# Performance work log

Hardware: AMD Instinct MI355X
Metric: run time of the kernel (lower is better)

Reference implementation:

```python
import jax, jax.numpy as jnp
import numpy as np

B = 2048   # batch size
D = 2048   # feature dim (ResNet-50)
H = 2048   # projection hidden dim
T = 0.1    # temperature
EPS_BN = 1e-5
CC_ITERS = 32  # >= ~2*log2(B), enough for pointer-jumping convergence


def setup_inputs() -> dict:
    key = jax.random.key(0)
    ks = jax.random.split(key, 4)
    s = 0.02
    return {
        "x1": jax.random.normal(ks[0], (B, D), dtype=jnp.float32),
        "x2": jax.random.normal(ks[1], (B, D), dtype=jnp.float32),
        "W1": jax.random.normal(ks[2], (H, D), dtype=jnp.float32) * s,
        "b1": jnp.zeros((H,), jnp.float32),
        "gamma": jnp.ones((H,), jnp.float32),
        "beta": jnp.zeros((H,), jnp.float32),
        "W2": jax.random.normal(ks[3], (D, H), dtype=jnp.float32) * s,
        "b2": jnp.zeros((D,), jnp.float32),
    }


def _head(x, W1, b1, gamma, beta, W2, b2):
    # ProjectionHead: Linear -> BatchNorm1d (train mode, batch stats) -> ReLU -> Linear
    h = x @ W1.T + b1
    mu = h.mean(0)
    var = h.var(0)  # biased variance, as torch BN uses for normalization
    h = (h - mu) * jax.lax.rsqrt(var + EPS_BN) * gamma + beta
    h = jax.nn.relu(h)
    o = h @ W2.T + b2
    n = jnp.maximum(jnp.linalg.norm(o, axis=1, keepdims=True), 1e-12)
    return o / n  # F.normalize


def _cc_mask(feat):
    # build_connected_component: kNN(k=1) graph + connected components -> same-label mask
    b = feat.shape[0]
    sim = jax.lax.stop_gradient(feat @ feat.T) - 2.0 * jnp.eye(b, dtype=feat.dtype)
    y = jnp.argmax(sim, axis=1)  # topk(1) neighbor per row
    # min-label propagation with pointer jumping (GPU-native union-find equivalent)
    def body(_, l):
        ln = jnp.minimum(l, l[y])      # propagate along edge i -> y[i]
        ln = ln.at[y].min(l)           # propagate along reverse edge y[i] -> i
        return jnp.minimum(ln, ln[ln])  # pointer jumping
    labels = jax.lax.fori_loop(0, CC_ITERS, body, jnp.arange(b))
    return (labels[:, None] == labels[None, :]).astype(feat.dtype)


def _sup_contra(logits, mask, diag):
    dm = 1.0 - diag
    mask = mask * dm
    exp_logits = jnp.exp(logits) * dm
    log_prob = logits - jnp.log(exp_logits.sum(1, keepdims=True))
    mean_log_prob_pos = (mask * log_prob).sum(1) / mask.sum(1)
    return (-mean_log_prob_pos).mean()


def reference(x1, x2, W1, b1, gamma, beta, W2, b2):
    # Only head2 branch contributes to the returned graph_loss (head1 branch is dead code
    # w.r.t. the return value), so we compute exactly the graph_loss path.
    feat1 = _head(x1, W1, b1, gamma, beta, W2, b2)
    feat2 = _head(x2, W1, b1, gamma, beta, W2, b2)
    mask1 = _cc_mask(feat1)
    mask2 = _cc_mask(feat2)
    diag = jnp.eye(B, dtype=feat1.dtype)
    loss = _sup_contra(feat1 @ feat1.T / T, mask2, diag)
    loss = loss + _sup_contra(feat2 @ feat2.T / T, mask1, diag)
    return loss / 2.0
```

## Files before the change

kernel.cpp:

```cpp
#include <hip/hip_runtime.h>
#include <hip/hip_bf16.h>

typedef __bf16 bf16_t;
typedef __bf16 bf16x4 __attribute__((ext_vector_type(4)));
typedef __bf16 bf16x8 __attribute__((ext_vector_type(8)));
typedef float  f32x4  __attribute__((ext_vector_type(4)));

__device__ __forceinline__ void gload_lds16(const void* g, void* l)
{
    __builtin_amdgcn_global_load_lds((__attribute__((address_space(1))) void*)g,
                                     (__attribute__((address_space(3))) void*)l,
                                     16, 0, 0);
}

__global__ __launch_bounds__(256) void cast_all(const float* __restrict__ x1, const float* __restrict__ x2,
                                                const float* __restrict__ W1, const float* __restrict__ W2,
                                                bf16_t* __restrict__ xcatb, bf16_t* __restrict__ W1b,
                                                bf16_t* __restrict__ W2b)
{
    const size_t i  = ((size_t)blockIdx.x * 256 + threadIdx.x) * 4;
    const size_t M4 = 1ull << 22;
    const size_t r  = i >> 22;
    const size_t off = i & (M4 - 1);
    const float* src; bf16_t* dst;
    if (r == 0)      { src = x1; dst = xcatb; }
    else if (r == 1) { src = x2; dst = xcatb + M4; }
    else if (r == 2) { src = W1; dst = W1b; }
    else             { src = W2; dst = W2b; }
    f32x4 v = *(const f32x4*)(src + off);
    bf16x4 o;
    o[0] = (bf16_t)v[0]; o[1] = (bf16_t)v[1]; o[2] = (bf16_t)v[2]; o[3] = (bf16_t)v[3];
    *(bf16x4*)(dst + off) = o;
}

__global__ __launch_bounds__(256) void gemm_bt(
    const bf16_t* __restrict__ A, const bf16_t* __restrict__ B,
    const float* __restrict__ bias, void* __restrict__ Cv,
    int N, int K, int rows_per_batch, long long b_batch_stride,
    int mode, int c_bf16,
    float* __restrict__ ps, float* __restrict__ ps2,
    float* __restrict__ rsq, const float* __restrict__ rnv,
    unsigned long long* __restrict__ pkey, float* __restrict__ lseP)
{
    __shared__ bf16_t lsA[128 * 64];
    __shared__ bf16_t lsB[128 * 64];
    __shared__ float  cs2[4][64];
    __shared__ float  cq2[4][64];
    __shared__ float  rq2[4][64];
    __shared__ float  ls2[4][64];
    __shared__ unsigned long long kv2[4][64];
    const int tid  = threadIdx.x;
    const int lane = tid & 63;
    const int wave = tid >> 6;
    const int wm   = (wave >> 1) * 64;
    const int wn   = (wave & 1) * 64;
    const int m0   = blockIdx.y * 128;
    const int n0   = blockIdx.x * 128;
    const bf16_t* Bb = B + (long long)(m0 / rows_per_batch) * b_batch_stride;

    f32x4 acc[4][4] = {};

    const int srow = tid >> 3;
    const int scol = (tid & 7) * 8;
    for (int kt = 0; kt < K; kt += 64) {
#pragma unroll
        for (int i = 0; i < 4; ++i) {
            const int r = i * 32 + srow;
            gload_lds16(A  + (size_t)(m0 + r) * K + kt + scol, lsA + r * 64 + scol);
            gload_lds16(Bb + (size_t)(n0 + r) * K + kt + scol, lsB + r * 64 + scol);
        }
        __syncthreads();
#pragma unroll
        for (int ks = 0; ks < 2; ++ks) {
            const int kk = ks * 32 + (lane >> 4) * 8;
            bf16x8 af[4], bfr[4];
#pragma unroll
            for (int f = 0; f < 4; ++f) {
                af[f]  = *(const bf16x8*)&lsA[(wm + f * 16 + (lane & 15)) * 64 + kk];
                bfr[f] = *(const bf16x8*)&lsB[(wn + f * 16 + (lane & 15)) * 64 + kk];
            }
#pragma unroll
            for (int fm = 0; fm < 4; ++fm)
#pragma unroll
                for (int fn = 0; fn < 4; ++fn)
                    acc[fm][fn] = __builtin_amdgcn_mfma_f32_16x16x32_bf16(af[fm], bfr[fn], acc[fm][fn], 0, 0, 0);
        }
        __syncthreads();
    }

    if (mode == 2) {
        const int rnb = (m0 >> 11) * 2048;
#pragma unroll
        for (int fm = 0; fm < 4; ++fm) {
            const int mb = m0 + wm + fm * 16 + ((lane >> 4) << 2);
            const f32x4 rm = *(const f32x4*)&rnv[mb];
#pragma unroll
            for (int fn = 0; fn < 4; ++fn) {
                const float rc = rnv[rnb + n0 + wn + fn * 16 + (lane & 15)];
#pragma unroll
                for (int r = 0; r < 4; ++r)
                    acc[fm][fn][r] *= rm[r] * rc;
            }
        }
    }

#pragma unroll
    for (int fm = 0; fm < 4; ++fm) {
        const int rb = m0 + wm + fm * 16 + ((lane >> 4) << 2);
#pragma unroll
        for (int fn = 0; fn < 4; ++fn) {
            const int colg = n0 + wn + fn * 16 + (lane & 15);
            const float bv = bias ? bias[colg] : 0.0f;
            if (c_bf16) {
                bf16_t* Cb = (bf16_t*)Cv;
#pragma unroll
                for (int r = 0; r < 4; ++r)
                    Cb[(size_t)(rb + r) * N + colg] = (bf16_t)(acc[fm][fn][r] + bv);
            } else {
                float* Cf = (float*)Cv;
#pragma unroll
                for (int r = 0; r < 4; ++r)
                    Cf[(size_t)(rb + r) * N + colg] = acc[fm][fn][r] + bv;
            }
        }
    }

    if (mode == 1) {
#pragma unroll
        for (int fn = 0; fn < 4; ++fn) {
            const int cl = fn * 16 + (lane & 15);
            const float bv = bias[n0 + wn + cl];
            float s = 0.f, q = 0.f;
#pragma unroll
            for (int fm = 0; fm < 4; ++fm)
#pragma unroll
                for (int r = 0; r < 4; ++r) {
                    const float v = acc[fm][fn][r] + bv;
                    s += v; q += v * v;
                }
            s += __shfl_xor(s, 16); q += __shfl_xor(q, 16);
            s += __shfl_xor(s, 32); q += __shfl_xor(q, 32);
            if (lane < 16) { cs2[wave][cl] = s; cq2[wave][cl] = q; }
        }
        __syncthreads();
        if (tid < 128) {
            const int wlo = (tid < 64) ? 0 : 1;
            const int cl  = tid & 63;
            ps [(size_t)blockIdx.y * 2048 + n0 + tid] = cs2[wlo][cl] + cs2[wlo + 2][cl];
            ps2[(size_t)blockIdx.y * 2048 + n0 + tid] = cq2[wlo][cl] + cq2[wlo + 2][cl];
        }
    } else if (mode == 3) {
#pragma unroll
        for (int fm = 0; fm < 4; ++fm)
#pragma unroll
            for (int r = 0; r < 4; ++r) {
                float q = 0.f;
#pragma unroll
                for (int fn = 0; fn < 4; ++fn) {
                    const float v = acc[fm][fn][r] + bias[n0 + wn + fn * 16 + (lane & 15)];
                    q += v * v;
                }
                q += __shfl_xor(q, 1); q += __shfl_xor(q, 2);
                q += __shfl_xor(q, 4); q += __shfl_xor(q, 8);
                if ((lane & 15) == 0)
                    rq2[wave][fm * 16 + ((lane >> 4) << 2) + r] = q;
            }
        __syncthreads();
        if (tid < 128) {
            const int wlo = (tid < 64) ? 0 : 2;
            const int rl  = tid & 63;
            rsq[(size_t)blockIdx.x * 4096 + m0 + tid] = rq2[wlo][rl] + rq2[wlo + 1][rl];
        }
    } else if (mode == 2) {
#pragma unroll
        for (int fm = 0; fm < 4; ++fm)
#pragma unroll
            for (int r = 0; r < 4; ++r) {
                const int rl   = fm * 16 + ((lane >> 4) << 2) + r;
                const int self = (m0 + wm + rl) & 2047;
                float best = -1.0e38f; int bi = 0x7fffffff; float se = 0.f;
#pragma unroll
                for (int fn = 0; fn < 4; ++fn) {
                    const int cg = n0 + wn + fn * 16 + (lane & 15);
                    const float v = acc[fm][fn][r];
                    if (cg != self) {
                        se += expf(10.0f * v);
                        if (v > best) { best = v; bi = cg; }
                    }
                }
#pragma unroll
                for (int st = 1; st <= 8; st <<= 1) {
                    const float ov = __shfl_xor(best, st);
                    const int   oi = __shfl_xor(bi, st);
                    if (ov > best || (ov == best && oi < bi)) { best = ov; bi = oi; }
                    se += __shfl_xor(se, st);
                }
                if ((lane & 15) == 0) {
                    unsigned u = __float_as_uint(best);
                    u = (u & 0x80000000u) ? ~u : (u | 0x80000000u);
                    kv2[wave][rl] = ((unsigned long long)u << 32) | (unsigned)(~bi);
                    ls2[wave][rl] = se;
                }
            }
        __syncthreads();
        if (tid < 128) {
            const int wlo = (tid < 64) ? 0 : 2;
            const int rl  = tid & 63;
            const unsigned long long a = kv2[wlo][rl], b = kv2[wlo + 1][rl];
            pkey[(size_t)blockIdx.x * 4096 + m0 + tid] = a > b ? a : b;
            lseP[(size_t)blockIdx.x * 4096 + m0 + tid] = ls2[wlo][rl] + ls2[wlo + 1][rl];
        }
    }
}

__global__ __launch_bounds__(256) void bn_final2(const float* __restrict__ ps, const float* __restrict__ ps2,
                                                 float* __restrict__ mu, float* __restrict__ rinv)
{
    const int c = blockIdx.x * 256 + threadIdx.x;
    const int b = c >> 11, col = c & 2047;
    float s = 0.f, s2 = 0.f;
    for (int i = 0; i < 16; ++i) {
        s  += ps [(size_t)(b * 16 + i) * 2048 + col];
        s2 += ps2[(size_t)(b * 16 + i) * 2048 + col];
    }
    const float m = s * (1.0f / 2048.0f);
    const float v = s2 * (1.0f / 2048.0f) - m * m;
    mu[c]   = m;
    rinv[c] = rsqrtf(v + 1e-5f);
}

__global__ __launch_bounds__(256) void bn_apply(const bf16_t* __restrict__ h, const float* __restrict__ mu,
                                                const float* __restrict__ rinv, const float* __restrict__ gamma,
                                                const float* __restrict__ beta, bf16_t* __restrict__ out)
{
    const size_t base = ((size_t)blockIdx.x * 256 + threadIdx.x) * 8;
    const int col = (int)(base & 2047);
    const int br  = (int)(base >> 22);
    bf16x8 v = *(const bf16x8*)(h + base);
    bf16x8 o;
#pragma unroll
    for (int j = 0; j < 8; ++j) {
        const int c = col + j;
        const float f = (float)v[j];
        const float t = (f - mu[br * 2048 + c]) * rinv[br * 2048 + c] * gamma[c] + beta[c];
        o[j] = (bf16_t)fmaxf(t, 0.0f);
    }
    *(bf16x8*)(out + base) = o;
}

__global__ __launch_bounds__(256) void norm_final(const float* __restrict__ rsq, float* __restrict__ rn)
{
    const int r = blockIdx.x * 256 + threadIdx.x;
    float s = 0.f;
    for (int nb = 0; nb < 16; ++nb) s += rsq[(size_t)nb * 4096 + r];
    rn[r] = 1.0f / fmaxf(sqrtf(s), 1e-12f);
}

__global__ __launch_bounds__(1024) void cc_labels(const unsigned long long* __restrict__ pkey,
                                                  int* __restrict__ labg)
{
    __shared__ int A_[2048];
    __shared__ int Bn[2048];
    __shared__ int Y_[2048];
    __shared__ int chg;
    const int br = blockIdx.x;
    const int t = threadIdx.x;
    if (t == 0) chg = 0;
    for (int i = t; i < 2048; i += 1024) {
        const int row = br * 2048 + i;
        unsigned long long k = 0ull;
        for (int nb = 0; nb < 16; ++nb) {
            const unsigned long long v = pkey[(size_t)nb * 4096 + row];
            k = (v > k) ? v : k;
        }
        Y_[i] = (int)~((unsigned)(k & 0xFFFFFFFFull));
        A_[i] = i;
    }
    __syncthreads();
    for (int it = 0; it < 32; ++it) {
        for (int i = t; i < 2048; i += 1024) Bn[i] = min(A_[i], A_[Y_[i]]);
        __syncthreads();
        for (int i = t; i < 2048; i += 1024) atomicMin(&Bn[Y_[i]], A_[i]);
        __syncthreads();
        int ch = 0;
        for (int i = t; i < 2048; i += 1024) {
            const int b = Bn[i];
            const int nv = min(b, Bn[b]);
            if (nv != A_[i]) { ch = 1; A_[i] = nv; }
        }
        if (ch) atomicOr(&chg, 1);
        __syncthreads();
        const int c = chg;
        __syncthreads();
        if (t == 0) chg = 0;
        if (!c) break;
    }
    for (int i = t; i < 2048; i += 1024) labg[br * 2048 + i] = A_[i];
}

__global__ __launch_bounds__(256) void loss_rows(const bf16_t* __restrict__ simb, const int* __restrict__ labels,
                                                 const float* __restrict__ lseP, float* __restrict__ terms)
{
    const int row = blockIdx.x;
    const int br  = row >> 11;
    const int* lab = labels + ((1 - br) << 11);
    const int self = row & 2047;
    const int li = lab[self];
    const int t = threadIdx.x;
    const bf16x8 v8 = *(const bf16x8*)(simb + (size_t)row * 2048 + t * 8);
    float psum = 0.f; int pc = 0;
#pragma unroll
    for (int j = 0; j < 8; ++j) {
        const int c = t * 8 + j;
        if (c == self) continue;
        if (lab[c] == li) { psum += 10.0f * (float)v8[j]; pc++; }
    }
    __shared__ float PS[256]; __shared__ int PC[256];
    PS[t] = psum; PC[t] = pc;
    __syncthreads();
    for (int off = 128; off; off >>= 1) {
        if (t < off) { PS[t] += PS[t + off]; PC[t] += PC[t + off]; }
        __syncthreads();
    }
    if (t == 0) {
        float se = 0.f;
        for (int nb = 0; nb < 16; ++nb) se += lseP[(size_t)nb * 4096 + row];
        terms[row] = logf(se) - PS[0] / (float)PC[0];
    }
}

__global__ __launch_bounds__(1024) void final_reduce(const float* __restrict__ terms, float* __restrict__ out)
{
    const int t = threadIdx.x;
    float s = terms[t] + terms[t + 1024] + terms[t + 2048] + terms[t + 3072];
    __shared__ float S[1024];
    S[t] = s;
    __syncthreads();
    for (int off = 512; off; off >>= 1) { if (t < off) S[t] += S[t + off]; __syncthreads(); }
    if (t == 0) out[0] = S[0] * (1.0f / 4096.0f);
}

extern "C" void kernel_launch(void* const* d_in, const int* in_sizes, int n_in,
                              void* d_out, int out_size, void* d_ws, size_t ws_size,
                              hipStream_t stream)
{
    const float* x1    = (const float*)d_in[0];
    const float* x2    = (const float*)d_in[1];
    const float* W1    = (const float*)d_in[2];
    const float* b1    = (const float*)d_in[3];
    const float* gamma = (const float*)d_in[4];
    const float* beta  = (const float*)d_in[5];
    const float* W2    = (const float*)d_in[6];
    const float* b2    = (const float*)d_in[7];

    char* ws = (char*)d_ws;
    const size_t MB = 1024ull * 1024ull;
    const size_t NN = 2048ull * 2048ull;
    bf16_t* W1b    = (bf16_t*)(ws + 0);
    bf16_t* W2b    = (bf16_t*)(ws + 8 * MB);
    bf16_t* xcatb  = (bf16_t*)(ws + 16 * MB);
    bf16_t* hnb    = (bf16_t*)(ws + 16 * MB);
    bf16_t* hb16   = (bf16_t*)(ws + 32 * MB);
    bf16_t* ob16   = (bf16_t*)(ws + 64 * MB);
    bf16_t* simb   = (bf16_t*)(ws + 0);
    float*  psA    = (float*)(ws + 80 * MB);
    float*  psB    = psA + 32 * 2048;
    float*  rsq    = psB + 32 * 2048;
    float*  mu     = rsq + 16 * 4096;
    float*  rinv   = mu + 4096;
    float*  rn     = rinv + 4096;
    float*  lseP   = rn + 4096;
    unsigned long long* pkey = (unsigned long long*)(lseP + 16 * 4096);
    int*    labels = (int*)(pkey + 16 * 4096);
    float*  terms  = (float*)(labels + 4096);

    cast_all<<<16384, 256, 0, stream>>>(x1, x2, W1, W2, xcatb, W1b, W2b);

    gemm_bt<<<dim3(16, 32), 256, 0, stream>>>(xcatb, W1b, b1, hb16, 2048, 2048, 1 << 30, 0,
                                              1, 1, psA, psB, nullptr, nullptr, nullptr, nullptr);
    bn_final2<<<16, 256, 0, stream>>>(psA, psB, mu, rinv);
    bn_apply<<<4096, 256, 0, stream>>>(hb16, mu, rinv, gamma, beta, hnb);

    gemm_bt<<<dim3(16, 32), 256, 0, stream>>>(hnb, W2b, b2, ob16, 2048, 2048, 1 << 30, 0,
                                              3, 1, nullptr, nullptr, rsq, nullptr, nullptr, nullptr);
    norm_final<<<16, 256, 0, stream>>>(rsq, rn);

    gemm_bt<<<dim3(16, 32), 256, 0, stream>>>(ob16, ob16, nullptr, simb, 2048, 2048, 2048, (long long)NN,
                                              2, 1, nullptr, nullptr, nullptr, rn, pkey, lseP);

    cc_labels<<<2, 1024, 0, stream>>>(pkey, labels);
    loss_rows<<<4096, 256, 0, stream>>>(simb, labels, lseP, terms);
    final_reduce<<<1, 1024, 0, stream>>>(terms, (float*)d_out);
}
```

Measured before the change: 238.8 us.

## Add 256x256-tile 8-wave pipelined GEMM for the first projection layer

Replaces the generic 128x128 gemm_bt for the first linear layer (4096x2048x2048) with a dedicated 512-thread kernel that uses 256x256 tiles, a 4-stage LDS ring of K=32 slices with XOR swizzle, and interleaved global-to-LDS prefetch with MFMA blocks under barriers and setprio. Larger tiles raise arithmetic intensity and the deeper pipeline is meant to hide load latency. The BN partial-sum reduction moves into the new kernel, and bn_final2 now sums 8 row-block partials instead of 16. The costs are 128 blocks on a large GPU (under one wave of CUs), higher register pressure, and a schedule that relies on hand-tuned waitcnt counts.

```diff
diff --git a/kernel.cpp b/kernel.cpp
--- a/kernel.cpp
+++ b/kernel.cpp
@@ -33,19 +33,162 @@
     *(bf16x4*)(dst + off) = o;
 }
 
+__global__ __launch_bounds__(512, 2) void gemm8(
+    const bf16_t* __restrict__ A, const bf16_t* __restrict__ B,
+    const float* __restrict__ bias, bf16_t* __restrict__ C,
+    float* __restrict__ ps, float* __restrict__ ps2)
+{
+    __shared__ bf16_t lsA[4][256 * 32];
+    __shared__ bf16_t lsB[4][256 * 32];
+    __shared__ float  cs2[8][64], cq2[8][64];
+    const int tid  = threadIdx.x;
+    const int lane = tid & 63;
+    const int wave = tid >> 6;
+    const int l15  = lane & 15;
+    const int cg   = lane >> 4;
+    const int wm   = (wave >> 2) * 128;
+    const int wn   = (wave & 3) * 64;
+    const int m0   = blockIdx.y * 256;
+    const int n0   = blockIdx.x * 256;
+    const int K = 2048, N = 2048, NT = 32;
+
+    f32x4 acc[8][4] = {};
+
+    auto STAGE = [&](const bf16_t* __restrict__ G, int row0, int k0, bf16_t* dst) {
+#pragma unroll
+        for (int i = 0; i < 2; ++i) {
+            const int ch  = wave * 128 + i * 64 + lane;
+            const int row = ch >> 2;
+            const int cs  = (ch & 3) ^ (row & 3);
+            gload_lds16(G + (size_t)(row0 + row) * K + k0 + cs * 8,
+                        dst + wave * 1024 + i * 512 + lane * 8);
+        }
+    };
+    auto FRAG = [&](const bf16_t* u, int row) -> bf16x8 {
+        return *(const bf16x8*)&u[row * 32 + ((cg ^ (row & 3)) << 3)];
+    };
+    auto LOADA = [&](const bf16_t* uA, int g, bf16x8* af) {
+#pragma unroll
+        for (int j = 0; j < 4; ++j) af[j] = FRAG(uA, wm + (g * 4 + j) * 16 + l15);
+    };
+    auto LOADB = [&](const bf16_t* uB, bf16x8* bfr) {
+#pragma unroll
+        for (int j = 0; j < 4; ++j) bfr[j] = FRAG(uB, wn + j * 16 + l15);
+    };
+    auto DOMFMA = [&](int g, bf16x8* af, bf16x8* bfr) {
+        __builtin_amdgcn_s_setprio(1);
+#pragma unroll
+        for (int j = 0; j < 4; ++j)
+#pragma unroll
+            for (int fn = 0; fn < 4; ++fn)
+                acc[g * 4 + j][fn] =
+                    __builtin_amdgcn_mfma_f32_16x16x32_bf16(af[j], bfr[fn], acc[g * 4 + j][fn], 0, 0, 0);
+        __builtin_amdgcn_s_setprio(0);
+    };
+
+    STAGE(A, m0, 0,  lsA[0]);
+    STAGE(B, n0, 0,  lsB[0]);
+    STAGE(A, m0, 32, lsA[1]);
+    STAGE(B, n0, 32, lsB[1]);
+    asm volatile("s_waitcnt vmcnt(4)" ::: "memory");
+    __builtin_amdgcn_sched_barrier(0);
+    __builtin_amdgcn_s_barrier();
+
+    for (int t = 0; t < NT; ++t) {
+        const int s0 = (2 * t) & 3, s1 = (2 * t + 1) & 3;
+        const int s2 = (2 * t + 2) & 3, s3 = (2 * t + 3) & 3;
+        const bool st = (t < NT - 1);
+        const int kn = (t + 1) * 64;
+        bf16x8 af[4], bfr[4];
+
+        LOADB(lsB[s0], bfr);
+        LOADA(lsA[s0], 0, af);
+        if (st) STAGE(A, m0, kn, lsA[s2]);
+        __builtin_amdgcn_sched_barrier(0);
+        __builtin_amdgcn_s_barrier();
+        __builtin_amdgcn_sched_barrier(0);
+        DOMFMA(0, af, bfr);
+        __builtin_amdgcn_sched_barrier(0);
+        __builtin_amdgcn_s_barrier();
+
+        LOADA(lsA[s0], 1, af);
+        if (st) { STAGE(B, n0, kn, lsB[s2]);
+                  asm volatile("s_waitcnt vmcnt(4)" ::: "memory"); }
+        else      asm volatile("s_waitcnt vmcnt(0)" ::: "memory");
+        __builtin_amdgcn_sched_barrier(0);
+        __builtin_amdgcn_s_barrier();
+        __builtin_amdgcn_sched_barrier(0);
+        DOMFMA(1, af, bfr);
+        __builtin_amdgcn_sched_barrier(0);
+        __builtin_amdgcn_s_barrier();
+
+        LOADB(lsB[s1], bfr);
+        LOADA(lsA[s1], 0, af);
+        if (st) STAGE(A, m0, kn + 32, lsA[s3]);
+        __builtin_amdgcn_sched_barrier(0);
+        __builtin_amdgcn_s_barrier();
+        __builtin_amdgcn_sched_barrier(0);
+        DOMFMA(0, af, bfr);
+        __builtin_amdgcn_sched_barrier(0);
+        __builtin_amdgcn_s_barrier();
+
+        LOADA(lsA[s1], 1, af);
+        if (st) { STAGE(B, n0, kn + 32, lsB[s3]);
+                  asm volatile("s_waitcnt vmcnt(4)" ::: "memory"); }
+        __builtin_amdgcn_sched_barrier(0);
+        __builtin_amdgcn_s_barrier();
+        __builtin_amdgcn_sched_barrier(0);
+        DOMFMA(1, af, bfr);
+        __builtin_amdgcn_sched_barrier(0);
+        __builtin_amdgcn_s_barrier();
+    }
+
+#pragma unroll
+    for (int fm = 0; fm < 8; ++fm) {
+        const int rb = m0 + wm + fm * 16 + ((lane >> 4) << 2);
+#pragma unroll
+        for (int fn = 0; fn < 4; ++fn) {
+            const int colg = n0 + wn + fn * 16 + l15;
+            const float bv = bias[colg];
+#pragma unroll
+            for (int r = 0; r < 4; ++r)
+                C[(size_t)(rb + r) * N + colg] = (bf16_t)(acc[fm][fn][r] + bv);
+        }
+    }
+#pragma unroll
+    for (int fn = 0; fn < 4; ++fn) {
+        const int cl = fn * 16 + l15;
+        const float bv = bias[n0 + wn + cl];
+        float s = 0.f, q = 0.f;
+#pragma unroll
+        for (int fm = 0; fm < 8; ++fm)
+#pragma unroll
+            for (int r = 0; r < 4; ++r) {
+                const float v = acc[fm][fn][r] + bv;
+                s += v; q += v * v;
+            }
+        s += __shfl_xor(s, 16); q += __shfl_xor(q, 16);
+        s += __shfl_xor(s, 32); q += __shfl_xor(q, 32);
+        if (lane < 16) { cs2[wave][cl] = s; cq2[wave][cl] = q; }
+    }
+    __syncthreads();
+    if (tid < 256) {
+        const int qn = tid >> 6, cl = tid & 63;
+        ps [(size_t)blockIdx.y * 2048 + n0 + tid] = cs2[qn][cl] + cs2[qn + 4][cl];
+        ps2[(size_t)blockIdx.y * 2048 + n0 + tid] = cq2[qn][cl] + cq2[qn + 4][cl];
+    }
+}
+
 __global__ __launch_bounds__(256) void gemm_bt(
     const bf16_t* __restrict__ A, const bf16_t* __restrict__ B,
     const float* __restrict__ bias, void* __restrict__ Cv,
     int N, int K, int rows_per_batch, long long b_batch_stride,
     int mode, int c_bf16,
-    float* __restrict__ ps, float* __restrict__ ps2,
     float* __restrict__ rsq, const float* __restrict__ rnv,
     unsigned long long* __restrict__ pkey, float* __restrict__ lseP)
 {
     __shared__ bf16_t lsA[128 * 64];
     __shared__ bf16_t lsB[128 * 64];
-    __shared__ float  cs2[4][64];
-    __shared__ float  cq2[4][64];
     __shared__ float  rq2[4][64];
     __shared__ float  ls2[4][64];
     __shared__ unsigned long long kv2[4][64];
@@ -125,31 +268,7 @@
         }
     }
 
-    if (mode == 1) {
-#pragma unroll
-        for (int fn = 0; fn < 4; ++fn) {
-            const int cl = fn * 16 + (lane & 15);
-            const float bv = bias[n0 + wn + cl];
-            float s = 0.f, q = 0.f;
-#pragma unroll
-            for (int fm = 0; fm < 4; ++fm)
-#pragma unroll
-                for (int r = 0; r < 4; ++r) {
-                    const float v = acc[fm][fn][r] + bv;
-                    s += v; q += v * v;
-                }
-            s += __shfl_xor(s, 16); q += __shfl_xor(q, 16);
-            s += __shfl_xor(s, 32); q += __shfl_xor(q, 32);
-            if (lane < 16) { cs2[wave][cl] = s; cq2[wave][cl] = q; }
-        }
-        __syncthreads();
-        if (tid < 128) {
-            const int wlo = (tid < 64) ? 0 : 1;
-            const int cl  = tid & 63;
-            ps [(size_t)blockIdx.y * 2048 + n0 + tid] = cs2[wlo][cl] + cs2[wlo + 2][cl];
-            ps2[(size_t)blockIdx.y * 2048 + n0 + tid] = cq2[wlo][cl] + cq2[wlo + 2][cl];
-        }
-    } else if (mode == 3) {
+    if (mode == 3) {
 #pragma unroll
         for (int fm = 0; fm < 4; ++fm)
 #pragma unroll
@@ -219,9 +338,9 @@
     const int c = blockIdx.x * 256 + threadIdx.x;
     const int b = c >> 11, col = c & 2047;
     float s = 0.f, s2 = 0.f;
-    for (int i = 0; i < 16; ++i) {
-        s  += ps [(size_t)(b * 16 + i) * 2048 + col];
-        s2 += ps2[(size_t)(b * 16 + i) * 2048 + col];
+    for (int i = 0; i < 8; ++i) {
+        s  += ps [(size_t)(b * 8 + i) * 2048 + col];
+        s2 += ps2[(size_t)(b * 8 + i) * 2048 + col];
     }
     const float m = s * (1.0f / 2048.0f);
     const float v = s2 * (1.0f / 2048.0f) - m * m;
@@ -376,17 +495,16 @@
 
     cast_all<<<16384, 256, 0, stream>>>(x1, x2, W1, W2, xcatb, W1b, W2b);
 
-    gemm_bt<<<dim3(16, 32), 256, 0, stream>>>(xcatb, W1b, b1, hb16, 2048, 2048, 1 << 30, 0,
-                                              1, 1, psA, psB, nullptr, nullptr, nullptr, nullptr);
+    gemm8<<<dim3(8, 16), 512, 0, stream>>>(xcatb, W1b, b1, hb16, psA, psB);
     bn_final2<<<16, 256, 0, stream>>>(psA, psB, mu, rinv);
     bn_apply<<<4096, 256, 0, stream>>>(hb16, mu, rinv, gamma, beta, hnb);
 
     gemm_bt<<<dim3(16, 32), 256, 0, stream>>>(hnb, W2b, b2, ob16, 2048, 2048, 1 << 30, 0,
-                                              3, 1, nullptr, nullptr, rsq, nullptr, nullptr, nullptr);
+                                              3, 1, rsq, nullptr, nullptr, nullptr);
     norm_final<<<16, 256, 0, stream>>>(rsq, rn);
 
     gemm_bt<<<dim3(16, 32), 256, 0, stream>>>(ob16, ob16, nullptr, simb, 2048, 2048, 2048, (long long)NN,
-                                              2, 1, nullptr, nullptr, nullptr, rn, pkey, lseP);
+                                              2, 1, nullptr, rn, pkey, lseP);
 
     cc_labels<<<2, 1024, 0, stream>>>(pkey, labels);
     loss_rows<<<4096, 256, 0, stream>>>(simb, labels, lseP, terms);
```

After: 264.0 us. +10.5%, slower.

## Rewrite GEMM as 8-wave 256x128 tile with 4-stage pipelined swizzled LDS

Applied to the files above, without the earlier changes.

Replaces the 4-wave 128x128 GEMM with an 8-wave kernel over a 256x128 tile. It uses a 4-slot ring of K=32 LDS buffers loaded asynchronously ahead of compute, with XOR-style swizzled LDS addressing to avoid bank conflicts, and raises wave priority around the MFMA blocks. The goal is to overlap global loads with MFMA work and cut the stall at each K-step barrier. In exchange it halves the grid to 256 blocks, which is about one block per CU, and it hardcodes K=N=2048. The epilogue reductions and the BN partial-sum count are adjusted to the new tile shape.

```diff
diff --git a/kernel.cpp b/kernel.cpp
--- a/kernel.cpp
+++ b/kernel.cpp
@@ -33,70 +33,116 @@
     *(bf16x4*)(dst + off) = o;
 }
 
-__global__ __launch_bounds__(256) void gemm_bt(
+__global__ __launch_bounds__(512, 1) void gemm8b(
     const bf16_t* __restrict__ A, const bf16_t* __restrict__ B,
-    const float* __restrict__ bias, void* __restrict__ Cv,
-    int N, int K, int rows_per_batch, long long b_batch_stride,
-    int mode, int c_bf16,
+    const float* __restrict__ bias, bf16_t* __restrict__ C,
+    long long b_batch_stride, int mode,
     float* __restrict__ ps, float* __restrict__ ps2,
     float* __restrict__ rsq, const float* __restrict__ rnv,
     unsigned long long* __restrict__ pkey, float* __restrict__ lseP)
 {
-    __shared__ bf16_t lsA[128 * 64];
-    __shared__ bf16_t lsB[128 * 64];
-    __shared__ float  cs2[4][64];
-    __shared__ float  cq2[4][64];
-    __shared__ float  rq2[4][64];
-    __shared__ float  ls2[4][64];
-    __shared__ unsigned long long kv2[4][64];
+    __shared__ bf16_t lsA[4][256 * 32];
+    __shared__ bf16_t lsB[4][128 * 32];
+    __shared__ float  cs2[8][64], cq2[8][64];
+    __shared__ float  rq2[8][64];
+    __shared__ float  ls2[8][64];
+    __shared__ unsigned long long kv2[8][64];
     const int tid  = threadIdx.x;
     const int lane = tid & 63;
     const int wave = tid >> 6;
+    const int l15  = lane & 15;
+    const int cg   = lane >> 4;
     const int wm   = (wave >> 1) * 64;
     const int wn   = (wave & 1) * 64;
-    const int m0   = blockIdx.y * 128;
+    const int m0   = blockIdx.y * 256;
     const int n0   = blockIdx.x * 128;
-    const bf16_t* Bb = B + (long long)(m0 / rows_per_batch) * b_batch_stride;
+    const int K = 2048, N = 2048, NT = 32;
+    const bf16_t* Bb = B + (size_t)(m0 >> 11) * b_batch_stride;
 
     f32x4 acc[4][4] = {};
 
-    const int srow = tid >> 3;
-    const int scol = (tid & 7) * 8;
-    for (int kt = 0; kt < K; kt += 64) {
-#pragma unroll
-        for (int i = 0; i < 4; ++i) {
-            const int r = i * 32 + srow;
-            gload_lds16(A  + (size_t)(m0 + r) * K + kt + scol, lsA + r * 64 + scol);
-            gload_lds16(Bb + (size_t)(n0 + r) * K + kt + scol, lsB + r * 64 + scol);
-        }
-        __syncthreads();
-#pragma unroll
-        for (int ks = 0; ks < 2; ++ks) {
-            const int kk = ks * 32 + (lane >> 4) * 8;
-            bf16x8 af[4], bfr[4];
-#pragma unroll
-            for (int f = 0; f < 4; ++f) {
-                af[f]  = *(const bf16x8*)&lsA[(wm + f * 16 + (lane & 15)) * 64 + kk];
-                bfr[f] = *(const bf16x8*)&lsB[(wn + f * 16 + (lane & 15)) * 64 + kk];
-            }
-#pragma unroll
-            for (int fm = 0; fm < 4; ++fm)
-#pragma unroll
-                for (int fn = 0; fn < 4; ++fn)
-                    acc[fm][fn] = __builtin_amdgcn_mfma_f32_16x16x32_bf16(af[fm], bfr[fn], acc[fm][fn], 0, 0, 0);
-        }
-        __syncthreads();
+    auto STAGE_A = [&](int k0, bf16_t* dst) {
+#pragma unroll
+        for (int i = 0; i < 2; ++i) {
+            const int ch  = wave * 128 + i * 64 + lane;
+            const int row = ch >> 2;
+            const int cs  = ((ch & 3) - ((row >> 1) & 3)) & 3;
+            gload_lds16(A + (size_t)(m0 + row) * K + k0 + cs * 8, dst + ch * 8);
+        }
+    };
+    auto STAGE_B = [&](int k0, bf16_t* dst) {
+        const int ch  = wave * 64 + lane;
+        const int row = ch >> 2;
+        const int cs  = ((ch & 3) - ((row >> 1) & 3)) & 3;
+        gload_lds16(Bb + (size_t)(n0 + row) * K + k0 + cs * 8, dst + ch * 8);
+    };
+    auto FRAG = [&](const bf16_t* u, int row) -> bf16x8 {
+        const int p = (cg + (row >> 1)) & 3;
+        return *(const bf16x8*)&u[row * 32 + p * 8];
+    };
+
+    STAGE_A(0,  lsA[0]); STAGE_B(0,  lsB[0]);
+    STAGE_A(32, lsA[1]); STAGE_B(32, lsB[1]);
+    asm volatile("s_waitcnt vmcnt(3)" ::: "memory");
+    __builtin_amdgcn_sched_barrier(0);
+    __builtin_amdgcn_s_barrier();
+
+    for (int t = 0; t < NT; ++t) {
+        const int s0 = (2 * t) & 3, s1 = (2 * t + 1) & 3;
+        const int s2 = (2 * t + 2) & 3, s3 = (2 * t + 3) & 3;
+        const bool st = (t < NT - 1);
+        const int kn = (t + 1) * 64;
+        bf16x8 af[4], bfr[4];
+
+#pragma unroll
+        for (int f = 0; f < 4; ++f) af[f]  = FRAG(lsA[s0], wm + f * 16 + l15);
+#pragma unroll
+        for (int f = 0; f < 4; ++f) bfr[f] = FRAG(lsB[s0], wn + f * 16 + l15);
+        if (st) { STAGE_A(kn, lsA[s2]); STAGE_B(kn, lsB[s2]);
+                  asm volatile("s_waitcnt vmcnt(3)" ::: "memory"); }
+        else      asm volatile("s_waitcnt vmcnt(0)" ::: "memory");
+        __builtin_amdgcn_sched_barrier(0);
+        __builtin_amdgcn_s_barrier();
+        __builtin_amdgcn_sched_barrier(0);
+        __builtin_amdgcn_s_setprio(1);
+#pragma unroll
+        for (int fm = 0; fm < 4; ++fm)
+#pragma unroll
+            for (int fn = 0; fn < 4; ++fn)
+                acc[fm][fn] = __builtin_amdgcn_mfma_f32_16x16x32_bf16(af[fm], bfr[fn], acc[fm][fn], 0, 0, 0);
+        __builtin_amdgcn_s_setprio(0);
+        __builtin_amdgcn_sched_barrier(0);
+        __builtin_amdgcn_s_barrier();
+
+#pragma unroll
+        for (int f = 0; f < 4; ++f) af[f]  = FRAG(lsA[s1], wm + f * 16 + l15);
+#pragma unroll
+        for (int f = 0; f < 4; ++f) bfr[f] = FRAG(lsB[s1], wn + f * 16 + l15);
+        if (st) { STAGE_A(kn + 32, lsA[s3]); STAGE_B(kn + 32, lsB[s3]);
+                  asm volatile("s_waitcnt vmcnt(3)" ::: "memory"); }
+        __builtin_amdgcn_sched_barrier(0);
+        __builtin_amdgcn_s_barrier();
+        __builtin_amdgcn_sched_barrier(0);
+        __builtin_amdgcn_s_setprio(1);
+#pragma unroll
+        for (int fm = 0; fm < 4; ++fm)
+#pragma unroll
+            for (int fn = 0; fn < 4; ++fn)
+                acc[fm][fn] = __builtin_amdgcn_mfma_f32_16x16x32_bf16(af[fm], bfr[fn], acc[fm][fn], 0, 0, 0);
+        __builtin_amdgcn_s_setprio(0);
+        __builtin_amdgcn_sched_barrier(0);
+        __builtin_amdgcn_s_barrier();
     }
 
     if (mode == 2) {
         const int rnb = (m0 >> 11) * 2048;
 #pragma unroll
         for (int fm = 0; fm < 4; ++fm) {
-            const int mb = m0 + wm + fm * 16 + ((lane >> 4) << 2);
+            const int mb = m0 + wm + fm * 16 + cg * 4;
             const f32x4 rm = *(const f32x4*)&rnv[mb];
 #pragma unroll
             for (int fn = 0; fn < 4; ++fn) {
-                const float rc = rnv[rnb + n0 + wn + fn * 16 + (lane & 15)];
+                const float rc = rnv[rnb + n0 + wn + fn * 16 + l15];
 #pragma unroll
                 for (int r = 0; r < 4; ++r)
                     acc[fm][fn][r] *= rm[r] * rc;
@@ -106,29 +152,21 @@
 
 #pragma unroll
     for (int fm = 0; fm < 4; ++fm) {
-        const int rb = m0 + wm + fm * 16 + ((lane >> 4) << 2);
+        const int rb = m0 + wm + fm * 16 + cg * 4;
 #pragma unroll
         for (int fn = 0; fn < 4; ++fn) {
-            const int colg = n0 + wn + fn * 16 + (lane & 15);
+            const int colg = n0 + wn + fn * 16 + l15;
             const float bv = bias ? bias[colg] : 0.0f;
-            if (c_bf16) {
-                bf16_t* Cb = (bf16_t*)Cv;
-#pragma unroll
-                for (int r = 0; r < 4; ++r)
-                    Cb[(size_t)(rb + r) * N + colg] = (bf16_t)(acc[fm][fn][r] + bv);
-            } else {
-                float* Cf = (float*)Cv;
-#pragma unroll
-                for (int r = 0; r < 4; ++r)
-                    Cf[(size_t)(rb + r) * N + colg] = acc[fm][fn][r] + bv;
-            }
+#pragma unroll
+            for (int r = 0; r < 4; ++r)
+                C[(size_t)(rb + r) * N + colg] = (bf16_t)(acc[fm][fn][r] + bv);
         }
     }
 
     if (mode == 1) {
 #pragma unroll
         for (int fn = 0; fn < 4; ++fn) {
-            const int cl = fn * 16 + (lane & 15);
+            const int cl = fn * 16 + l15;
             const float bv = bias[n0 + wn + cl];
             float s = 0.f, q = 0.f;
 #pragma unroll
@@ -144,10 +182,11 @@
         }
         __syncthreads();
         if (tid < 128) {
-            const int wlo = (tid < 64) ? 0 : 1;
-            const int cl  = tid & 63;
-            ps [(size_t)blockIdx.y * 2048 + n0 + tid] = cs2[wlo][cl] + cs2[wlo + 2][cl];
-            ps2[(size_t)blockIdx.y * 2048 + n0 + tid] = cq2[wlo][cl] + cq2[wlo + 2][cl];
+            const int p = tid >> 6, cl = tid & 63;
+            ps [(size_t)blockIdx.y * 2048 + n0 + tid] =
+                cs2[p][cl] + cs2[p + 2][cl] + cs2[p + 4][cl] + cs2[p + 6][cl];
+            ps2[(size_t)blockIdx.y * 2048 + n0 + tid] =
+                cq2[p][cl] + cq2[p + 2][cl] + cq2[p + 4][cl] + cq2[p + 6][cl];
         }
     } else if (mode == 3) {
 #pragma unroll
@@ -157,45 +196,43 @@
                 float q = 0.f;
 #pragma unroll
                 for (int fn = 0; fn < 4; ++fn) {
-                    const float v = acc[fm][fn][r] + bias[n0 + wn + fn * 16 + (lane & 15)];
+                    const float v = acc[fm][fn][r] + bias[n0 + wn + fn * 16 + l15];
                     q += v * v;
                 }
                 q += __shfl_xor(q, 1); q += __shfl_xor(q, 2);
                 q += __shfl_xor(q, 4); q += __shfl_xor(q, 8);
-                if ((lane & 15) == 0)
-                    rq2[wave][fm * 16 + ((lane >> 4) << 2) + r] = q;
+                if (l15 == 0) rq2[wave][fm * 16 + cg * 4 + r] = q;
             }
         __syncthreads();
-        if (tid < 128) {
-            const int wlo = (tid < 64) ? 0 : 2;
-            const int rl  = tid & 63;
-            rsq[(size_t)blockIdx.x * 4096 + m0 + tid] = rq2[wlo][rl] + rq2[wlo + 1][rl];
+        if (tid < 256) {
+            const int mg = tid >> 6, rl = tid & 63;
+            rsq[(size_t)blockIdx.x * 4096 + m0 + tid] = rq2[2 * mg][rl] + rq2[2 * mg + 1][rl];
         }
     } else if (mode == 2) {
 #pragma unroll
         for (int fm = 0; fm < 4; ++fm)
 #pragma unroll
             for (int r = 0; r < 4; ++r) {
-                const int rl   = fm * 16 + ((lane >> 4) << 2) + r;
+                const int rl   = fm * 16 + cg * 4 + r;
                 const int self = (m0 + wm + rl) & 2047;
                 float best = -1.0e38f; int bi = 0x7fffffff; float se = 0.f;
 #pragma unroll
                 for (int fn = 0; fn < 4; ++fn) {
-                    const int cg = n0 + wn + fn * 16 + (lane & 15);
+                    const int cgl = n0 + wn + fn * 16 + l15;
                     const float v = acc[fm][fn][r];
-                    if (cg != self) {
+                    if (cgl != self) {
                         se += expf(10.0f * v);
-                        if (v > best) { best = v; bi = cg; }
+                        if (v > best) { best = v; bi = cgl; }
                     }
                 }
 #pragma unroll
-                for (int st = 1; st <= 8; st <<= 1) {
-                    const float ov = __shfl_xor(best, st);
-                    const int   oi = __shfl_xor(bi, st);
+                for (int st2 = 1; st2 <= 8; st2 <<= 1) {
+                    const float ov = __shfl_xor(best, st2);
+                    const int   oi = __shfl_xor(bi, st2);
                     if (ov > best || (ov == best && oi < bi)) { best = ov; bi = oi; }
-                    se += __shfl_xor(se, st);
+                    se += __shfl_xor(se, st2);
                 }
-                if ((lane & 15) == 0) {
+                if (l15 == 0) {
                     unsigned u = __float_as_uint(best);
                     u = (u & 0x80000000u) ? ~u : (u | 0x80000000u);
                     kv2[wave][rl] = ((unsigned long long)u << 32) | (unsigned)(~bi);
@@ -203,12 +240,11 @@
                 }
             }
         __syncthreads();
-        if (tid < 128) {
-            const int wlo = (tid < 64) ? 0 : 2;
-            const int rl  = tid & 63;
-            const unsigned long long a = kv2[wlo][rl], b = kv2[wlo + 1][rl];
+        if (tid < 256) {
+            const int mg = tid >> 6, rl = tid & 63;
+            const unsigned long long a = kv2[2 * mg][rl], b = kv2[2 * mg + 1][rl];
             pkey[(size_t)blockIdx.x * 4096 + m0 + tid] = a > b ? a : b;
-            lseP[(size_t)blockIdx.x * 4096 + m0 + tid] = ls2[wlo][rl] + ls2[wlo + 1][rl];
+            lseP[(size_t)blockIdx.x * 4096 + m0 + tid] = ls2[2 * mg][rl] + ls2[2 * mg + 1][rl];
         }
     }
 }
@@ -219,9 +255,9 @@
     const int c = blockIdx.x * 256 + threadIdx.x;
     const int b = c >> 11, col = c & 2047;
     float s = 0.f, s2 = 0.f;
-    for (int i = 0; i < 16; ++i) {
-        s  += ps [(size_t)(b * 16 + i) * 2048 + col];
-        s2 += ps2[(size_t)(b * 16 + i) * 2048 + col];
+    for (int i = 0; i < 8; ++i) {
+        s  += ps [(size_t)(b * 8 + i) * 2048 + col];
+        s2 += ps2[(size_t)(b * 8 + i) * 2048 + col];
     }
     const float m = s * (1.0f / 2048.0f);
     const float v = s2 * (1.0f / 2048.0f) - m * m;
@@ -376,17 +412,17 @@
 
     cast_all<<<16384, 256, 0, stream>>>(x1, x2, W1, W2, xcatb, W1b, W2b);
 
-    gemm_bt<<<dim3(16, 32), 256, 0, stream>>>(xcatb, W1b, b1, hb16, 2048, 2048, 1 << 30, 0,
-                                              1, 1, psA, psB, nullptr, nullptr, nullptr, nullptr);
+    gemm8b<<<dim3(16, 16), 512, 0, stream>>>(xcatb, W1b, b1, hb16, 0, 1,
+                                             psA, psB, nullptr, nullptr, nullptr, nullptr);
     bn_final2<<<16, 256, 0, stream>>>(psA, psB, mu, rinv);
     bn_apply<<<4096, 256, 0, stream>>>(hb16, mu, rinv, gamma, beta, hnb);
 
-    gemm_bt<<<dim3(16, 32), 256, 0, stream>>>(hnb, W2b, b2, ob16, 2048, 2048, 1 << 30, 0,
-                                              3, 1, nullptr, nullptr, rsq, nullptr, nullptr, nullptr);
+    gemm8b<<<dim3(16, 16), 512, 0, stream>>>(hnb, W2b, b2, ob16, 0, 3,
+                                             nullptr, nullptr, rsq, nullptr, nullptr, nullptr);
     norm_final<<<16, 256, 0, stream>>>(rsq, rn);
 
-    gemm_bt<<<dim3(16, 32), 256, 0, stream>>>(ob16, ob16, nullptr, simb, 2048, 2048, 2048, (long long)NN,
-                                              2, 1, nullptr, nullptr, nullptr, rn, pkey, lseP);
+    gemm8b<<<dim3(16, 16), 512, 0, stream>>>(ob16, ob16, nullptr, simb, (long long)NN, 2,
+                                             nullptr, nullptr, nullptr, rn, pkey, lseP);
 
     cc_labels<<<2, 1024, 0, stream>>>(pkey, labels);
     loss_rows<<<4096, 256, 0, stream>>>(simb, labels, lseP, terms);
```

New measurement: 216.4 us. -9.4%, faster.
